# Performance work log

Hardware: AMD Instinct MI355X
Metric: run time of the kernel (lower is better)

The kernel has to match this reference:

```python
import jax, jax.numpy as jnp
import numpy as np

B, L, T = 4, 512, 4096
HID, NH = 1024, 16
HD = HID // NH
MAX_POS = 4096
BASE = 10000.0


def _cos_sin(dim, max_pos, base):
    inv_freq = 1.0 / base ** (jnp.arange(0, dim, 2, dtype=jnp.float32) / dim)
    t = jnp.arange(max_pos, dtype=jnp.float32)
    freqs = jnp.einsum('i,j->ij', t, inv_freq)
    emb = jnp.concatenate([freqs, freqs], axis=-1)  # [max_pos, dim]
    return jnp.cos(emb), jnp.sin(emb)


def _rotate_half(x):
    x1, x2 = x[..., : x.shape[-1] // 2], x[..., x.shape[-1] // 2:]
    return jnp.concatenate([-x2, x1], axis=-1)


def setup_inputs() -> dict:
    key = jax.random.key(0)
    ks = jax.random.split(key, 12)
    s = 0.02
    inp = {
        'latents': jax.random.normal(ks[0], (B, L, HID), jnp.float32),
        'target': jax.random.normal(ks[1], (B, T, HID), jnp.float32),
        'target_mask': jax.random.randint(ks[2], (B, T), 0, 2).astype(bool),
        'target_timestamp': jnp.sort(jax.random.randint(ks[3], (B, T), 0, MAX_POS), axis=-1),
        'Wq': jax.random.normal(ks[4], (HID, HID), jnp.float32) * s,
        'bq': jnp.zeros((HID,), jnp.float32),
        'Wk': jax.random.normal(ks[5], (HID, HID), jnp.float32) * s,
        'bk': jnp.zeros((HID,), jnp.float32),
        'Wv': jax.random.normal(ks[6], (HID, HID), jnp.float32) * s,
        'bv': jnp.zeros((HID,), jnp.float32),
        'Wo': jax.random.normal(ks[7], (HID, HID), jnp.float32) * s,
        'bo': jnp.zeros((HID,), jnp.float32),
    }
    return inp


def reference(latents, target, target_mask, target_timestamp, Wq, bq, Wk, bk, Wv, bv, Wo, bo):
    cos, sin = _cos_sin(HD, MAX_POS, BASE)  # [MAX_POS, HD]
    # latents_timestamp: arange(L) * (max-1)/(L-1), cast to int
    lat_ts = (jnp.arange(L, dtype=jnp.float32) * (MAX_POS - 1) / (L - 1)).astype(jnp.int64)
    lat_ts = jnp.broadcast_to(lat_ts[None, :], (B, L))

    # QKV projections (torch Linear: x @ W.T + b)
    q = (latents @ Wq.T + bq).reshape(B, L, NH, HD).transpose(0, 2, 1, 3)  # [B,H,L,D]
    k = (target @ Wk.T + bk).reshape(B, T, NH, HD).transpose(0, 2, 1, 3)   # [B,H,T,D]
    v = (target @ Wv.T + bv).reshape(B, T, NH, HD).transpose(0, 2, 1, 3)

    # RoPE with gathered timestamps; unsqueeze over head dim
    cq, sq = cos[lat_ts][:, None], sin[lat_ts][:, None]          # [B,1,L,D]
    ck, sk = cos[target_timestamp][:, None], sin[target_timestamp][:, None]  # [B,1,T,D]
    q = q * cq + _rotate_half(q) * sq
    k = k * ck + _rotate_half(k) * sk

    # SDPA with boolean attn mask (True = attend)
    scores = jnp.einsum('bhld,bhtd->bhlt', q, k) / jnp.sqrt(jnp.float32(HD))
    bias = jnp.where(target_mask[:, None, None, :], 0.0, -jnp.inf).astype(scores.dtype)
    attn = jax.nn.softmax(scores + bias, axis=-1)
    out = jnp.einsum('bhlt,bhtd->bhld', attn, v)  # [B,H,L,D]
    out = out.transpose(0, 2, 1, 3).reshape(B, L, HID)
    return out @ Wo.T + bo
```

## Files before the change

### kernel.cpp

```cpp
#include <hip/hip_runtime.h>

#define B_ 4
#define L_ 512
#define T_ 4096
#define NH_ 16
#define HD_ 64

using f32x4 = __attribute__((ext_vector_type(4))) float;
using bf16x8 = __attribute__((ext_vector_type(8))) short;
using u32x4 = __attribute__((ext_vector_type(4))) unsigned int;

__device__ __forceinline__ unsigned short f2bf(float x) {
  unsigned int u = __builtin_bit_cast(unsigned int, x);
  u += 0x7fffu + ((u >> 16) & 1u);
  return (unsigned short)(u >> 16);
}

__device__ __forceinline__ unsigned cvtpk(float lo, float hi) {
  unsigned r;
  asm("v_cvt_pk_bf16_f32 %0, %1, %2" : "=v"(r) : "v"(lo), "v"(hi));
  return r;
}

__device__ __forceinline__ u32x4 cvt8(const float4& a, const float4& b) {
  u32x4 r;
  r[0] = (unsigned)f2bf(a.x) | ((unsigned)f2bf(a.y) << 16);
  r[1] = (unsigned)f2bf(a.z) | ((unsigned)f2bf(a.w) << 16);
  r[2] = (unsigned)f2bf(b.x) | ((unsigned)f2bf(b.y) << 16);
  r[3] = (unsigned)f2bf(b.z) | ((unsigned)f2bf(b.w) << 16);
  return r;
}

__device__ __forceinline__ void gload16(const void* g, void* l) {
  __builtin_amdgcn_global_load_lds(
      (const __attribute__((address_space(1))) unsigned int*)g,
      (__attribute__((address_space(3))) unsigned int*)l, 16, 0, 0);
}

#define BC8(x) __builtin_bit_cast(bf16x8, (x))

struct CvtArgs {
  const float* src[6];
  unsigned short* dst[6];
  int cum[7];
};

__global__ void cvt_bf16(CvtArgs a, int total) {
  for (int g = blockIdx.x * 256 + threadIdx.x; g < total; g += gridDim.x * 256) {
    int r = 0;
#pragma unroll
    for (int q = 0; q < 5; ++q) r += (g >= a.cum[q + 1]);
    const int lc = g - a.cum[r];
    const float4* s = (const float4*)a.src[r] + (size_t)lc * 2;
    float4 x0 = s[0], x1 = s[1];
    *((u32x4*)a.dst[r] + lc) = cvt8(x0, x1);
  }
}

__global__ void rope_table(float* __restrict__ cost, float* __restrict__ sint,
                           const int* __restrict__ mask, float* __restrict__ mbias) {
  const int idx = blockIdx.x * 256 + threadIdx.x;
  const int pos = idx >> 5, i = idx & 31;
  const float inv = 1.0f / powf(10000.0f, (float)(2 * i) * (1.0f / 64.0f));
  const float f = (float)pos * inv;
  cost[idx] = cosf(f);
  sint[idx] = sinf(f);
  if (idx < B_ * T_) mbias[idx] = mask[idx] ? 0.f : -1e30f;
}

template <int EPI>
__global__ __launch_bounds__(256, 2) void gemm_bf(
    const unsigned short* __restrict__ A, const unsigned short* __restrict__ Wb,
    const float* __restrict__ bias, void* __restrict__ outp,
    const float* __restrict__ cost, const float* __restrict__ sint,
    const int* __restrict__ ts) {
  __shared__ u32x4 lsA[2][512];
  __shared__ u32x4 lsB[2][512];
  const int tid = threadIdx.x;
  const int mt = blockIdx.x >> 3, nt = blockIdx.x & 7;
  const int mBase = mt << 7, nBase = nt << 7;
  const int lane = tid & 63, wid = tid >> 6;
  const int wr = wid >> 1, wc = wid & 1;
  const int lr = lane & 15, lg = lane >> 4;

  f32x4 acc[4][4];
#pragma unroll
  for (int m = 0; m < 4; ++m)
#pragma unroll
    for (int n = 0; n < 4; ++n) acc[m][n] = (f32x4){0.f, 0.f, 0.f, 0.f};

  auto stage = [&](int bi, int kt) {
    const int ko = kt * 32;
#pragma unroll
    for (int j2 = 0; j2 < 2; ++j2) {
      const int j = wid * 2 + j2;
      const int row = (j & 1) * 64 + lane;
      const int kg = j >> 1;
      gload16(A + (size_t)(mBase + row) * 1024 + ko + kg * 8,
              (unsigned short*)lsA[bi] + j * 512);
      gload16(Wb + (size_t)(nBase + row) * 1024 + ko + kg * 8,
              (unsigned short*)lsB[bi] + j * 512);
    }
  };

  stage(0, 0);
  __syncthreads();
  int cur = 0;
  for (int kt = 0; kt < 32; ++kt) {
    if (kt < 31) stage(cur ^ 1, kt + 1);
    const u32x4* As = lsA[cur];
    const u32x4* Bs = lsB[cur];
    bf16x8 af[4], bfr[4];
#pragma unroll
    for (int m = 0; m < 4; ++m) af[m] = BC8(As[lg * 128 + wr * 64 + m * 16 + lr]);
#pragma unroll
    for (int n = 0; n < 4; ++n) bfr[n] = BC8(Bs[lg * 128 + wc * 64 + n * 16 + lr]);
#pragma unroll
    for (int m = 0; m < 4; ++m)
#pragma unroll
      for (int n = 0; n < 4; ++n)
        acc[m][n] = __builtin_amdgcn_mfma_f32_16x16x32_bf16(af[m], bfr[n], acc[m][n], 0, 0, 0);
    __syncthreads();
    cur ^= 1;
  }

  float bv[4];
#pragma unroll
  for (int n = 0; n < 4; ++n) bv[n] = bias[nBase + wc * 64 + n * 16 + lr];

  if (EPI == 3) {
    float* Of = (float*)outp;
#pragma unroll
    for (int m = 0; m < 4; ++m)
#pragma unroll
      for (int r = 0; r < 4; ++r) {
        const int gR = mBase + wr * 64 + m * 16 + lg * 4 + r;
#pragma unroll
        for (int n = 0; n < 4; ++n)
          Of[(size_t)gR * 1024 + nBase + wc * 64 + n * 16 + lr] = acc[m][n][r] + bv[n];
      }
  } else {
    unsigned short* Qo = (unsigned short*)outp;
    const int h = (nBase >> 6) + wc;
#pragma unroll
    for (int m = 0; m < 4; ++m) {
#pragma unroll
      for (int r = 0; r < 4; ++r) {
        const int gR = mBase + wr * 64 + m * 16 + lg * 4 + r;
        const int b2 = gR >> 9, p2 = gR & 511;
        const int pos = (int)(((float)p2 * 4095.0f) / 511.0f);
        const float* cp = cost + pos * 32;
        const float* sp = sint + pos * 32;
        const size_t obase = (((size_t)(b2 * NH_ + h)) * L_ + p2) * HD_;
#pragma unroll
        for (int n = 0; n < 2; ++n) {
          const int d = n * 16 + lr;
          const float x1 = acc[m][n][r] + bv[n];
          const float x2 = acc[m][n + 2][r] + bv[n + 2];
          const float c = cp[d], s = sp[d];
          Qo[obase + d] = f2bf(x1 * c - x2 * s);
          Qo[obase + d + 32] = f2bf(x2 * c + x1 * s);
        }
      }
    }
  }
}

__global__ __launch_bounds__(256, 2) void gemm_kv(
    const unsigned short* __restrict__ A, const unsigned short* __restrict__ Wkb,
    const unsigned short* __restrict__ Wvb, const float* __restrict__ bkp,
    const float* __restrict__ bvp, unsigned short* __restrict__ Ko,
    unsigned short* __restrict__ Vo, const float* __restrict__ cost,
    const float* __restrict__ sint, const int* __restrict__ ts) {
  __shared__ u32x4 lsA[2][512];
  __shared__ u32x4 lsK[2][512];
  __shared__ u32x4 lsV[2][512];
  const int tid = threadIdx.x;
  const int orig = blockIdx.x;
  const int wgid = (orig & 7) * 128 + (orig >> 3);
  const int mt = wgid >> 3, nt = wgid & 7;
  const int mBase = mt << 7, nBase = nt << 7;
  const int lane = tid & 63, wid = tid >> 6;
  const int wr = wid >> 1, wc = wid & 1;
  const int lr = lane & 15, lg = lane >> 4;

  f32x4 accK[4][4], accV[4][4];
#pragma unroll
  for (int m = 0; m < 4; ++m)
#pragma unroll
    for (int n = 0; n < 4; ++n) {
      accK[m][n] = (f32x4){0.f, 0.f, 0.f, 0.f};
      accV[m][n] = (f32x4){0.f, 0.f, 0.f, 0.f};
    }

  auto stage = [&](int bi, int kt) {
    const int ko = kt * 32;
#pragma unroll
    for (int j2 = 0; j2 < 2; ++j2) {
      const int j = wid * 2 + j2;
      const int row = (j & 1) * 64 + lane;
      const int kg = j >> 1;
      gload16(A + (size_t)(mBase + row) * 1024 + ko + kg * 8,
              (unsigned short*)lsA[bi] + j * 512);
      gload16(Wkb + (size_t)(nBase + row) * 1024 + ko + kg * 8,
              (unsigned short*)lsK[bi] + j * 512);
      gload16(Wvb + (size_t)(nBase + row) * 1024 + ko + kg * 8,
              (unsigned short*)lsV[bi] + j * 512);
    }
  };

  stage(0, 0);
  __syncthreads();
  int cur = 0;
  for (int kt = 0; kt < 32; ++kt) {
    if (kt < 31) stage(cur ^ 1, kt + 1);
    const u32x4* As = lsA[cur];
    const u32x4* Ks = lsK[cur];
    const u32x4* Vs = lsV[cur];
    bf16x8 af[4], kf[4], vf[4];
#pragma unroll
    for (int m = 0; m < 4; ++m) af[m] = BC8(As[lg * 128 + wr * 64 + m * 16 + lr]);
#pragma unroll
    for (int n = 0; n < 4; ++n) kf[n] = BC8(Ks[lg * 128 + wc * 64 + n * 16 + lr]);
#pragma unroll
    for (int n = 0; n < 4; ++n) vf[n] = BC8(Vs[lg * 128 + wc * 64 + n * 16 + lr]);
#pragma unroll
    for (int m = 0; m < 4; ++m)
#pragma unroll
      for (int n = 0; n < 4; ++n) {
        accK[m][n] = __builtin_amdgcn_mfma_f32_16x16x32_bf16(af[m], kf[n], accK[m][n], 0, 0, 0);
        accV[m][n] = __builtin_amdgcn_mfma_f32_16x16x32_bf16(af[m], vf[n], accV[m][n], 0, 0, 0);
      }
    __syncthreads();
    cur ^= 1;
  }

  const int h = (nBase >> 6) + wc;
  float bk4[4], bv4[4];
#pragma unroll
  for (int n = 0; n < 4; ++n) {
    bk4[n] = bkp[nBase + wc * 64 + n * 16 + lr];
    bv4[n] = bvp[nBase + wc * 64 + n * 16 + lr];
  }
#pragma unroll
  for (int m = 0; m < 4; ++m) {
#pragma unroll
    for (int r = 0; r < 4; ++r) {
      const int gR = mBase + wr * 64 + m * 16 + lg * 4 + r;
      const int b2 = gR >> 12, p2 = gR & 4095;
      const int pos = ts[gR];
      const float* cp = cost + pos * 32;
      const float* sp = sint + pos * 32;
      const size_t obase = (((size_t)(b2 * NH_ + h)) * T_ + p2) * HD_;
#pragma unroll
      for (int n = 0; n < 2; ++n) {
        const int d = n * 16 + lr;
        const float x1 = accK[m][n][r] + bk4[n];
        const float x2 = accK[m][n + 2][r] + bk4[n + 2];
        const float c = cp[d], s = sp[d];
        Ko[obase + d] = f2bf(x1 * c - x2 * s);
        Ko[obase + d + 32] = f2bf(x2 * c + x1 * s);
      }
    }
  }
#pragma unroll
  for (int m = 0; m < 4; ++m) {
    const int r0 = mBase + wr * 64 + m * 16 + lg * 4;
    const int b = r0 >> 12, t = r0 & 4095;
#pragma unroll
    for (int n = 0; n < 4; ++n) {
      const int d = n * 16 + lr;
      ushort4 pk;
      pk.x = f2bf(accV[m][n][0] + bv4[n]);
      pk.y = f2bf(accV[m][n][1] + bv4[n]);
      pk.z = f2bf(accV[m][n][2] + bv4[n]);
      pk.w = f2bf(accV[m][n][3] + bv4[n]);
      *(ushort4*)(Vo + (((size_t)(b * NH_ + h)) * HD_ + d) * (size_t)T_ + t) = pk;
    }
  }
}

#define SCL 0.180336880111f
__global__ __launch_bounds__(256, 4) void attn_half(
    const unsigned short* __restrict__ Q, const unsigned short* __restrict__ K,
    const unsigned short* __restrict__ V, const float* __restrict__ mbias,
    float* __restrict__ pws, float* __restrict__ mlws) {
  __shared__ u32x4 QP[512];
  __shared__ u32x4 Ks[2][512];
  __shared__ u32x4 Vs[2][512];
  const int tid = threadIdx.x, lane = tid & 63, w = tid >> 6;
  const int lr = lane & 15, lg = lane >> 4;
  const int orig = blockIdx.x;
  const int wg = (orig & 7) * 128 + (orig >> 3);
  const int half = wg & 1, lt = (wg >> 1) & 7, bh = wg >> 4;
  const int b = bh >> 4;
  const int l0 = lt << 6;
  const int tBase = half << 11;

#pragma unroll
  for (int i = 0; i < 2; ++i) {
    const int li = w * 2 + i;
    gload16(Q + ((size_t)bh * L_ + l0 + lane) * HD_ + li * 8, (unsigned short*)QP + li * 512);
  }
  __syncthreads();
  bf16x8 qf[2];
#pragma unroll
  for (int ks2 = 0; ks2 < 2; ++ks2)
    qf[ks2] = BC8(QP[(ks2 * 4 + lg) * 64 + w * 16 + lr]);

  f32x4 po[4];
#pragma unroll
  for (int n = 0; n < 4; ++n) po[n] = (f32x4){0.f, 0.f, 0.f, 0.f};
  float mrun = -1e30f, lrun = 0.f;

  char* Pw = (char*)QP + w * 2048;
  const int swz = (lr & 7) << 4;
  const float* mrow = mbias + (size_t)b * T_ + tBase;

  auto stage = [&](int bi, int it) {
    const int t0 = tBase + (it << 6);
#pragma unroll
    for (int i = 0; i < 2; ++i) {
      const int li = w * 2 + i;
      gload16(K + ((size_t)bh * T_ + t0 + lane) * HD_ + li * 8, (unsigned short*)Ks[bi] + li * 512);
      gload16(V + ((size_t)bh * HD_ + lane) * T_ + t0 + li * 8, (unsigned short*)Vs[bi] + li * 512);
    }
  };

  stage(0, 0);
  __syncthreads();
  int cur = 0;
  for (int it = 0; it < 32; ++it) {
    if (it < 31) stage(cur ^ 1, it + 1);
    const int t0l = it << 6;

    f32x4 s[4];
#pragma unroll
    for (int n = 0; n < 4; ++n) s[n] = (f32x4){0.f, 0.f, 0.f, 0.f};
#pragma unroll
    for (int ks2 = 0; ks2 < 2; ++ks2) {
#pragma unroll
      for (int n = 0; n < 4; ++n) {
        bf16x8 kb = BC8(Ks[cur][(ks2 * 4 + lg) * 64 + n * 16 + lr]);
        s[n] = __builtin_amdgcn_mfma_f32_16x16x32_bf16(kb, qf[ks2], s[n], 0, 0, 0);
      }
    }
#pragma unroll
    for (int n = 0; n < 4; ++n) {
      const f32x4 mb = *(const f32x4*)(mrow + t0l + n * 16 + lg * 4);
#pragma unroll
      for (int r = 0; r < 4; ++r) s[n][r] = s[n][r] * SCL + mb[r];
    }
    f32x4 m4;
#pragma unroll
    for (int r = 0; r < 4; ++r)
      m4[r] = fmaxf(fmaxf(s[0][r], s[1][r]), fmaxf(s[2][r], s[3][r]));
    float x = fmaxf(fmaxf(m4[0], m4[1]), fmaxf(m4[2], m4[3]));
    x = fmaxf(x, __shfl_xor(x, 16));
    x = fmaxf(x, __shfl_xor(x, 32));
    const float mnew = fmaxf(mrun, x);
    const float sc = __builtin_exp2f(mrun - mnew);
    mrun = mnew;
    f32x4 ls4 = (f32x4){0.f, 0.f, 0.f, 0.f};
#pragma unroll
    for (int n = 0; n < 4; ++n)
#pragma unroll
      for (int r = 0; r < 4; ++r) {
        const float p = __builtin_exp2f(s[n][r] - mnew);
        s[n][r] = p;
        ls4[r] += p;
      }
    lrun = lrun * sc + ((ls4[0] + ls4[1]) + (ls4[2] + ls4[3]));
#pragma unroll
    for (int n = 0; n < 4; ++n) po[n] *= sc;
#pragma unroll
    for (int n = 0; n < 4; ++n) {
      uint2 pk;
      pk.x = cvtpk(s[n][0], s[n][1]);
      pk.y = cvtpk(s[n][2], s[n][3]);
      *(uint2*)(Pw + ((lr * 128 + n * 32 + lg * 8) ^ swz)) = pk;
    }
    bf16x8 pa[2];
#pragma unroll
    for (int ks2 = 0; ks2 < 2; ++ks2)
      pa[ks2] = BC8(*(const u32x4*)(Pw + ((lr * 128 + ks2 * 64 + lg * 16) ^ swz)));
#pragma unroll
    for (int ks2 = 0; ks2 < 2; ++ks2) {
#pragma unroll
      for (int n = 0; n < 4; ++n) {
        bf16x8 vb = BC8(Vs[cur][(ks2 * 4 + lg) * 64 + n * 16 + lr]);
        po[n] = __builtin_amdgcn_mfma_f32_16x16x32_bf16(vb, pa[ks2], po[n], 0, 0, 0);
      }
    }
    __syncthreads();
    cur ^= 1;
  }

  lrun += __shfl_xor(lrun, 16);
  lrun += __shfl_xor(lrun, 32);
  const int l = w * 16 + lr;
  float* pbase = pws + ((size_t)(((bh << 3) + lt) * 2 + half)) * 4096;
  float* mlbase = mlws + ((size_t)(((bh << 3) + lt) * 2 + half)) * 128;
#pragma unroll
  for (int n = 0; n < 4; ++n)
    *(f32x4*)(pbase + l * 64 + n * 16 + lg * 4) = po[n];
  if (lg == 0) {
    mlbase[l * 2] = mrun;
    mlbase[l * 2 + 1] = lrun;
  }
}

__global__ void attn_combine(const float* __restrict__ pws, const float* __restrict__ mlws,
                             unsigned short* __restrict__ O) {
  const int blk = blockIdx.x;
  const int bh = blk >> 3, lt = blk & 7;
  const int b = bh >> 4, h = bh & 15;
  const int tid = threadIdx.x;
  const int row = tid >> 2, seg = tid & 3;
  const float* p0 = pws + ((size_t)blk * 2) * 4096 + row * 64 + seg * 16;
  const float* p1 = p0 + 4096;
  const float* ml0 = mlws + ((size_t)blk * 2) * 128 + row * 2;
  const float* ml1 = ml0 + 128;
  const float m0 = ml0[0], li0 = ml0[1], m1 = ml1[0], li1 = ml1[1];
  const float M = fmaxf(m0, m1);
  const float w0 = __builtin_exp2f(m0 - M), w1 = __builtin_exp2f(m1 - M);
  const float inv = 1.0f / (li0 * w0 + li1 * w1);
  const int gl = lt * 64 + row;
  unsigned short* orow = O + ((size_t)b * L_ + gl) * 1024 + h * HD_ + seg * 16;
#pragma unroll
  for (int j = 0; j < 4; ++j) {
    const float4 a = *(const float4*)(p0 + j * 4);
    const float4 c = *(const float4*)(p1 + j * 4);
    ushort4 pk;
    pk.x = f2bf((a.x * w0 + c.x * w1) * inv);
    pk.y = f2bf((a.y * w0 + c.y * w1) * inv);
    pk.z = f2bf((a.z * w0 + c.z * w1) * inv);
    pk.w = f2bf((a.w * w0 + c.w * w1) * inv);
    *(ushort4*)(orow + j * 4) = pk;
  }
}

extern "C" void kernel_launch(void* const* d_in, const int* in_sizes, int n_in,
                              void* d_out, int out_size, void* d_ws, size_t ws_size,
                              hipStream_t stream) {
  const float* latents = (const float*)d_in[0];
  const float* target = (const float*)d_in[1];
  const int* mask = (const int*)d_in[2];
  const int* ts = (const int*)d_in[3];
  const float* Wq = (const float*)d_in[4];
  const float* bq = (const float*)d_in[5];
  const float* Wk = (const float*)d_in[6];
  const float* bk = (const float*)d_in[7];
  const float* Wv = (const float*)d_in[8];
  const float* bv = (const float*)d_in[9];
  const float* Wo = (const float*)d_in[10];
  const float* bo = (const float*)d_in[11];
  float* out = (float*)d_out;

  char* ws = (char*)d_ws;
  float* cost = (float*)ws;
  float* sint = (float*)(ws + (512 << 10));
  unsigned short* Qws = (unsigned short*)(ws + (1ull << 20));
  unsigned short* Kws = (unsigned short*)(ws + (5ull << 20));
  unsigned short* Vws = (unsigned short*)(ws + (37ull << 20));
  float* mbias = (float*)(ws + (69ull << 20));
  unsigned short* Ows = (unsigned short*)(ws + (69ull << 20));
  unsigned short* latb = (unsigned short*)(ws + (73ull << 20));
  unsigned short* tgtb = (unsigned short*)(ws + (77ull << 20));
  float* pws = (float*)(ws + (77ull << 20));
  float* mlws = (float*)(ws + (93ull << 20));
  unsigned short* Wqb = (unsigned short*)(ws + (109ull << 20));
  unsigned short* Wkb = (unsigned short*)(ws + (111ull << 20));
  unsigned short* Wvb = (unsigned short*)(ws + (113ull << 20));
  unsigned short* Wob = (unsigned short*)(ws + (115ull << 20));

  CvtArgs ca;
  ca.src[0] = latents; ca.dst[0] = latb;
  ca.src[1] = target;  ca.dst[1] = tgtb;
  ca.src[2] = Wq;      ca.dst[2] = Wqb;
  ca.src[3] = Wk;      ca.dst[3] = Wkb;
  ca.src[4] = Wv;      ca.dst[4] = Wvb;
  ca.src[5] = Wo;      ca.dst[5] = Wob;
  const int nch[6] = {2097152 / 8, 16777216 / 8, 131072, 131072, 131072, 131072};
  ca.cum[0] = 0;
  for (int i = 0; i < 6; ++i) ca.cum[i + 1] = ca.cum[i] + nch[i];
  const int total = ca.cum[6];

  cvt_bf16<<<dim3(2048), dim3(256), 0, stream>>>(ca, total);
  rope_table<<<dim3(512), dim3(256), 0, stream>>>(cost, sint, mask, mbias);
  gemm_bf<0><<<dim3(16 * 8), dim3(256), 0, stream>>>(latb, Wqb, bq, Qws, cost, sint, nullptr);
  gemm_kv<<<dim3(1024), dim3(256), 0, stream>>>(tgtb, Wkb, Wvb, bk, bv, Kws, Vws, cost, sint, ts);
  attn_half<<<dim3(1024), dim3(256), 0, stream>>>(Qws, Kws, Vws, mbias, pws, mlws);
  attn_combine<<<dim3(512), dim3(256), 0, stream>>>(pws, mlws, Ows);
  gemm_bf<3><<<dim3(16 * 8), dim3(256), 0, stream>>>(Ows, Wob, bo, out, nullptr, nullptr, nullptr);
}
```

Measured before the change: 317.5 us.

## Fuse fp32-to-bf16 conversion of target into KV GEMM and split K/V tiles

After: 291.2 us. -8.3%, faster.

```diff
diff --git a/kernel.cpp b/kernel.cpp
--- a/kernel.cpp
+++ b/kernel.cpp
@@ -40,16 +40,16 @@
 #define BC8(x) __builtin_bit_cast(bf16x8, (x))
 
 struct CvtArgs {
-  const float* src[6];
-  unsigned short* dst[6];
-  int cum[7];
+  const float* src[5];
+  unsigned short* dst[5];
+  int cum[6];
 };
 
 __global__ void cvt_bf16(CvtArgs a, int total) {
   for (int g = blockIdx.x * 256 + threadIdx.x; g < total; g += gridDim.x * 256) {
     int r = 0;
 #pragma unroll
-    for (int q = 0; q < 5; ++q) r += (g >= a.cum[q + 1]);
+    for (int q = 0; q < 4; ++q) r += (g >= a.cum[q + 1]);
     const int lc = g - a.cum[r];
     const float4* s = (const float4*)a.src[r] + (size_t)lc * 2;
     float4 x0 = s[0], x1 = s[1];
@@ -166,116 +166,132 @@
   }
 }
 
-__global__ __launch_bounds__(256, 2) void gemm_kv(
-    const unsigned short* __restrict__ A, const unsigned short* __restrict__ Wkb,
-    const unsigned short* __restrict__ Wvb, const float* __restrict__ bkp,
-    const float* __restrict__ bvp, unsigned short* __restrict__ Ko,
-    unsigned short* __restrict__ Vo, const float* __restrict__ cost,
-    const float* __restrict__ sint, const int* __restrict__ ts) {
+__global__ __launch_bounds__(256, 3) void gemm_kv2(
+    const float* __restrict__ A, const unsigned short* __restrict__ Wkv,
+    const float* __restrict__ bkp, const float* __restrict__ bvp,
+    unsigned short* __restrict__ Ko, unsigned short* __restrict__ Vo,
+    const float* __restrict__ cost, const float* __restrict__ sint,
+    const int* __restrict__ ts) {
   __shared__ u32x4 lsA[2][512];
-  __shared__ u32x4 lsK[2][512];
-  __shared__ u32x4 lsV[2][512];
+  __shared__ u32x4 lsB[2][512];
   const int tid = threadIdx.x;
   const int orig = blockIdx.x;
-  const int wgid = (orig & 7) * 128 + (orig >> 3);
-  const int mt = wgid >> 3, nt = wgid & 7;
+  const int wgid = (orig & 7) * 256 + (orig >> 3);
+  const int mt = wgid >> 4, nt = wgid & 15;
   const int mBase = mt << 7, nBase = nt << 7;
   const int lane = tid & 63, wid = tid >> 6;
   const int wr = wid >> 1, wc = wid & 1;
   const int lr = lane & 15, lg = lane >> 4;
-
-  f32x4 accK[4][4], accV[4][4];
+  const int crow0 = tid >> 2, ckg = tid & 3;
+
+  f32x4 acc[4][4];
 #pragma unroll
   for (int m = 0; m < 4; ++m)
 #pragma unroll
-    for (int n = 0; n < 4; ++n) {
-      accK[m][n] = (f32x4){0.f, 0.f, 0.f, 0.f};
-      accV[m][n] = (f32x4){0.f, 0.f, 0.f, 0.f};
-    }
-
-  auto stage = [&](int bi, int kt) {
+    for (int n = 0; n < 4; ++n) acc[m][n] = (f32x4){0.f, 0.f, 0.f, 0.f};
+
+  const size_t arow0 = (size_t)(mBase + crow0) * 1024 + ckg * 8;
+  const size_t arow1 = (size_t)(mBase + crow0 + 64) * 1024 + ckg * 8;
+  const int dsti0 = ckg * 128 + crow0;
+  const int dsti1 = ckg * 128 + crow0 + 64;
+
+  auto stageW = [&](int bi, int kt) {
     const int ko = kt * 32;
 #pragma unroll
     for (int j2 = 0; j2 < 2; ++j2) {
       const int j = wid * 2 + j2;
       const int row = (j & 1) * 64 + lane;
       const int kg = j >> 1;
-      gload16(A + (size_t)(mBase + row) * 1024 + ko + kg * 8,
-              (unsigned short*)lsA[bi] + j * 512);
-      gload16(Wkb + (size_t)(nBase + row) * 1024 + ko + kg * 8,
-              (unsigned short*)lsK[bi] + j * 512);
-      gload16(Wvb + (size_t)(nBase + row) * 1024 + ko + kg * 8,
-              (unsigned short*)lsV[bi] + j * 512);
+      gload16(Wkv + (size_t)(nBase + row) * 1024 + ko + kg * 8,
+              (unsigned short*)lsB[bi] + j * 512);
     }
   };
 
-  stage(0, 0);
+  {
+    float4 x0 = *(const float4*)(A + arow0), x1 = *(const float4*)(A + arow0 + 4);
+    float4 x2 = *(const float4*)(A + arow1), x3 = *(const float4*)(A + arow1 + 4);
+    lsA[0][dsti0] = cvt8(x0, x1);
+    lsA[0][dsti1] = cvt8(x2, x3);
+    stageW(0, 0);
+  }
   __syncthreads();
   int cur = 0;
   for (int kt = 0; kt < 32; ++kt) {
-    if (kt < 31) stage(cur ^ 1, kt + 1);
+    float4 fa0, fa1, fa2, fa3;
+    const bool pre = (kt < 31);
+    if (pre) {
+      const int ko = (kt + 1) * 32;
+      fa0 = *(const float4*)(A + arow0 + ko);
+      fa1 = *(const float4*)(A + arow0 + ko + 4);
+      fa2 = *(const float4*)(A + arow1 + ko);
+      fa3 = *(const float4*)(A + arow1 + ko + 4);
+      stageW(cur ^ 1, kt + 1);
+    }
     const u32x4* As = lsA[cur];
-    const u32x4* Ks = lsK[cur];
-    const u32x4* Vs = lsV[cur];
-    bf16x8 af[4], kf[4], vf[4];
+    const u32x4* Bs = lsB[cur];
+    bf16x8 af[4], bfr[4];
 #pragma unroll
     for (int m = 0; m < 4; ++m) af[m] = BC8(As[lg * 128 + wr * 64 + m * 16 + lr]);
 #pragma unroll
-    for (int n = 0; n < 4; ++n) kf[n] = BC8(Ks[lg * 128 + wc * 64 + n * 16 + lr]);
-#pragma unroll
-    for (int n = 0; n < 4; ++n) vf[n] = BC8(Vs[lg * 128 + wc * 64 + n * 16 + lr]);
+    for (int n = 0; n < 4; ++n) bfr[n] = BC8(Bs[lg * 128 + wc * 64 + n * 16 + lr]);
 #pragma unroll
     for (int m = 0; m < 4; ++m)
 #pragma unroll
-      for (int n = 0; n < 4; ++n) {
-        accK[m][n] = __builtin_amdgcn_mfma_f32_16x16x32_bf16(af[m], kf[n], accK[m][n], 0, 0, 0);
-        accV[m][n] = __builtin_amdgcn_mfma_f32_16x16x32_bf16(af[m], vf[n], accV[m][n], 0, 0, 0);
-      }
+      for (int n = 0; n < 4; ++n)
+        acc[m][n] = __builtin_amdgcn_mfma_f32_16x16x32_bf16(af[m], bfr[n], acc[m][n], 0, 0, 0);
+    if (pre) {
+      lsA[cur ^ 1][dsti0] = cvt8(fa0, fa1);
+      lsA[cur ^ 1][dsti1] = cvt8(fa2, fa3);
+    }
     __syncthreads();
     cur ^= 1;
   }
 
-  const int h = (nBase >> 6) + wc;
-  float bk4[4], bv4[4];
-#pragma unroll
-  for (int n = 0; n < 4; ++n) {
-    bk4[n] = bkp[nBase + wc * 64 + n * 16 + lr];
-    bv4[n] = bvp[nBase + wc * 64 + n * 16 + lr];
-  }
-#pragma unroll
-  for (int m = 0; m < 4; ++m) {
-#pragma unroll
-    for (int r = 0; r < 4; ++r) {
-      const int gR = mBase + wr * 64 + m * 16 + lg * 4 + r;
-      const int b2 = gR >> 12, p2 = gR & 4095;
-      const int pos = ts[gR];
-      const float* cp = cost + pos * 32;
-      const float* sp = sint + pos * 32;
-      const size_t obase = (((size_t)(b2 * NH_ + h)) * T_ + p2) * HD_;
-#pragma unroll
-      for (int n = 0; n < 2; ++n) {
+  const bool isV = (nBase >= 1024);
+  const int nb = isV ? (nBase - 1024) : nBase;
+  const float* bp = isV ? bvp : bkp;
+  const int h = (nb >> 6) + wc;
+  float bb[4];
+#pragma unroll
+  for (int n = 0; n < 4; ++n) bb[n] = bp[nb + wc * 64 + n * 16 + lr];
+
+  if (!isV) {
+#pragma unroll
+    for (int m = 0; m < 4; ++m) {
+#pragma unroll
+      for (int r = 0; r < 4; ++r) {
+        const int gR = mBase + wr * 64 + m * 16 + lg * 4 + r;
+        const int b2 = gR >> 12, p2 = gR & 4095;
+        const int pos = ts[gR];
+        const float* cp = cost + pos * 32;
+        const float* sp = sint + pos * 32;
+        const size_t obase = (((size_t)(b2 * NH_ + h)) * T_ + p2) * HD_;
+#pragma unroll
+        for (int n = 0; n < 2; ++n) {
+          const int d = n * 16 + lr;
+          const float x1 = acc[m][n][r] + bb[n];
+          const float x2 = acc[m][n + 2][r] + bb[n + 2];
+          const float c = cp[d], s = sp[d];
+          Ko[obase + d] = f2bf(x1 * c - x2 * s);
+          Ko[obase + d + 32] = f2bf(x2 * c + x1 * s);
+        }
+      }
+    }
+  } else {
+#pragma unroll
+    for (int m = 0; m < 4; ++m) {
+      const int r0 = mBase + wr * 64 + m * 16 + lg * 4;
+      const int b = r0 >> 12, t = r0 & 4095;
+#pragma unroll
+      for (int n = 0; n < 4; ++n) {
         const int d = n * 16 + lr;
-        const float x1 = accK[m][n][r] + bk4[n];
-        const float x2 = accK[m][n + 2][r] + bk4[n + 2];
-        const float c = cp[d], s = sp[d];
-        Ko[obase + d] = f2bf(x1 * c - x2 * s);
-        Ko[obase + d + 32] = f2bf(x2 * c + x1 * s);
-      }
-    }
-  }
-#pragma unroll
-  for (int m = 0; m < 4; ++m) {
-    const int r0 = mBase + wr * 64 + m * 16 + lg * 4;
-    const int b = r0 >> 12, t = r0 & 4095;
-#pragma unroll
-    for (int n = 0; n < 4; ++n) {
-      const int d = n * 16 + lr;
-      ushort4 pk;
-      pk.x = f2bf(accV[m][n][0] + bv4[n]);
-      pk.y = f2bf(accV[m][n][1] + bv4[n]);
-      pk.z = f2bf(accV[m][n][2] + bv4[n]);
-      pk.w = f2bf(accV[m][n][3] + bv4[n]);
-      *(ushort4*)(Vo + (((size_t)(b * NH_ + h)) * HD_ + d) * (size_t)T_ + t) = pk;
+        ushort4 pk;
+        pk.x = f2bf(acc[m][n][0] + bb[n]);
+        pk.y = f2bf(acc[m][n][1] + bb[n]);
+        pk.z = f2bf(acc[m][n][2] + bb[n]);
+        pk.w = f2bf(acc[m][n][3] + bb[n]);
+        *(ushort4*)(Vo + (((size_t)(b * NH_ + h)) * HD_ + d) * (size_t)T_ + t) = pk;
+      }
     }
   }
 }
@@ -466,30 +482,27 @@
   float* mbias = (float*)(ws + (69ull << 20));
   unsigned short* Ows = (unsigned short*)(ws + (69ull << 20));
   unsigned short* latb = (unsigned short*)(ws + (73ull << 20));
-  unsigned short* tgtb = (unsigned short*)(ws + (77ull << 20));
   float* pws = (float*)(ws + (77ull << 20));
   float* mlws = (float*)(ws + (93ull << 20));
   unsigned short* Wqb = (unsigned short*)(ws + (109ull << 20));
-  unsigned short* Wkb = (unsigned short*)(ws + (111ull << 20));
-  unsigned short* Wvb = (unsigned short*)(ws + (113ull << 20));
+  unsigned short* Wkvb = (unsigned short*)(ws + (111ull << 20));
   unsigned short* Wob = (unsigned short*)(ws + (115ull << 20));
 
   CvtArgs ca;
   ca.src[0] = latents; ca.dst[0] = latb;
-  ca.src[1] = target;  ca.dst[1] = tgtb;
-  ca.src[2] = Wq;      ca.dst[2] = Wqb;
-  ca.src[3] = Wk;      ca.dst[3] = Wkb;
-  ca.src[4] = Wv;      ca.dst[4] = Wvb;
-  ca.src[5] = Wo;      ca.dst[5] = Wob;
-  const int nch[6] = {2097152 / 8, 16777216 / 8, 131072, 131072, 131072, 131072};
+  ca.src[1] = Wq;      ca.dst[1] = Wqb;
+  ca.src[2] = Wk;      ca.dst[2] = Wkvb;
+  ca.src[3] = Wv;      ca.dst[3] = Wkvb + (1 << 20);
+  ca.src[4] = Wo;      ca.dst[4] = Wob;
+  const int nch[5] = {2097152 / 8, 131072, 131072, 131072, 131072};
   ca.cum[0] = 0;
-  for (int i = 0; i < 6; ++i) ca.cum[i + 1] = ca.cum[i] + nch[i];
-  const int total = ca.cum[6];
-
-  cvt_bf16<<<dim3(2048), dim3(256), 0, stream>>>(ca, total);
+  for (int i = 0; i < 5; ++i) ca.cum[i + 1] = ca.cum[i] + nch[i];
+  const int total = ca.cum[5];
+
+  cvt_bf16<<<dim3(1024), dim3(256), 0, stream>>>(ca, total);
   rope_table<<<dim3(512), dim3(256), 0, stream>>>(cost, sint, mask, mbias);
   gemm_bf<0><<<dim3(16 * 8), dim3(256), 0, stream>>>(latb, Wqb, bq, Qws, cost, sint, nullptr);
-  gemm_kv<<<dim3(1024), dim3(256), 0, stream>>>(tgtb, Wkb, Wvb, bk, bv, Kws, Vws, cost, sint, ts);
+  gemm_kv2<<<dim3(2048), dim3(256), 0, stream>>>(target, Wkvb, bk, bv, Kws, Vws, cost, sint, ts);
   attn_half<<<dim3(1024), dim3(256), 0, stream>>>(Qws, Kws, Vws, mbias, pws, mlws);
   attn_combine<<<dim3(512), dim3(256), 0, stream>>>(pws, mlws, Ows);
   gemm_bf<3><<<dim3(16 * 8), dim3(256), 0, stream>>>(Ows, Wob, bo, out, nullptr, nullptr, nullptr);
```
